# Kernel optimization log

Measured on AMD Instinct MI355X. Metric: run time of the kernel, lower is better.

Reference implementation:

```python
import jax, jax.numpy as jnp
import numpy as np

# TT-linear: in_features=1024 -> out_features=4096
IN_DIMS = (8, 8, 4, 4)      # m1..m4, prod = 1024
OUT_DIMS = (8, 8, 8, 8)     # n1..n4, prod = 4096
RANKS = (1, 16, 16, 16, 1)  # r0..r4
IN_FEATURES = 1024
OUT_FEATURES = 4096
BATCH, SEQ = 4, 1024


def _init_core(key, shape):
    # uniform(-1,1)/sqrt(fan_in-ish), matching the original's uniform-style init scale
    fan = shape[0] * shape[1]
    return (2.0 * jax.random.uniform(key, shape, dtype=jnp.float32) - 1.0) / np.sqrt(fan).astype(np.float32)


def setup_inputs() -> dict:
    key = jax.random.key(0)
    ks = jax.random.split(key, 6)
    x = jax.random.normal(ks[0], (BATCH, SEQ, IN_FEATURES), dtype=jnp.float32)
    core0 = _init_core(ks[1], (1, 8, 8, 16))    # [r0, m1, n1, r1]
    core1 = _init_core(ks[2], (16, 8, 8, 16))   # [r1, m2, n2, r2]
    core2 = _init_core(ks[3], (16, 4, 8, 16))   # [r2, m3, n3, r3]
    core3 = _init_core(ks[4], (16, 4, 8, 1))    # [r3, m4, n4, r4]
    bias = (2.0 * jax.random.uniform(ks[5], (OUT_FEATURES,), dtype=jnp.float32) - 1.0) / np.sqrt(OUT_FEATURES).astype(np.float32)
    return {"x": x, "core0": core0, "core1": core1, "core2": core2, "core3": core3, "bias": bias}


def reference(x, core0, core1, core2, core3, bias):
    lead = x.shape[:-1]
    # split the feature axis into TT input factors: [T, m1, m2, m3, m4]
    t = x.reshape((-1,) + IN_DIMS)
    c0 = core0[0]        # [m1, n1, r1]   (boundary rank r0 = 1 squeezed)
    c3 = core3[..., 0]   # [r3, m4, n4]   (boundary rank r4 = 1 squeezed)
    # sequential TT core chain: absorb one m_k, emit one n_k per step
    t = jnp.einsum('tijkl,ixp->tjklxp', t, c0)      # [T, m2,m3,m4, n1, r1]
    t = jnp.einsum('tjklxp,pjyq->tklxyq', t, core1)  # [T, m3,m4, n1,n2, r2]
    t = jnp.einsum('tklxyq,qkzr->tlxyzr', t, core2)  # [T, m4, n1,n2,n3, r3]
    t = jnp.einsum('tlxyzr,rlw->txyzw', t, c3)       # [T, n1,n2,n3,n4]
    y = t.reshape(lead + (OUT_FEATURES,)) + bias
    return y
```

## Files before the change

kernel.cpp:

```cpp
#include <hip/hip_runtime.h>
#include <hip/hip_bf16.h>
#include <cstdint>


typedef __bf16 bf16x8 __attribute__((ext_vector_type(8)));
typedef float f32x4 __attribute__((ext_vector_type(4)));

__device__ __forceinline__ void g2lds16(const void* g, void* l) {
    __builtin_amdgcn_global_load_lds(
        (const __attribute__((address_space(1))) void*)g,
        (__attribute__((address_space(3))) void*)l,
        16, 0, 0);
}

__global__ void f32_to_bf16(const float* __restrict__ x, __bf16* __restrict__ y) {
    int i = (blockIdx.x * blockDim.x + threadIdx.x) * 8;
    float4 a = *(const float4*)(x + i);
    float4 b = *(const float4*)(x + i + 4);
    bf16x8 o;
    o[0] = (__bf16)a.x; o[1] = (__bf16)a.y; o[2] = (__bf16)a.z; o[3] = (__bf16)a.w;
    o[4] = (__bf16)b.x; o[5] = (__bf16)b.y; o[6] = (__bf16)b.z; o[7] = (__bf16)b.w;
    *(bf16x8*)(y + i) = o;
}

__global__ void build_wt(const float* __restrict__ c0, const float* __restrict__ c1,
                         const float* __restrict__ c2, const float* __restrict__ c3,
                         __bf16* __restrict__ wt) {
    __shared__ float t12[16];
    __shared__ float t123[4 * 8 * 16];
    const int b = blockIdx.x;
    const int m1 = b >> 9, n1 = (b >> 6) & 7, m2 = (b >> 3) & 7, n2 = b & 7;
    const int tid = threadIdx.x;
    if (tid < 16) {
        const int r2 = tid;
        float s = 0.f;
        #pragma unroll
        for (int r1 = 0; r1 < 16; ++r1)
            s += c0[(m1 * 8 + n1) * 16 + r1] * c1[((r1 * 8 + m2) * 8 + n2) * 16 + r2];
        t12[r2] = s;
    }
    __syncthreads();
    #pragma unroll
    for (int idx = tid; idx < 512; idx += 64) {
        const int m3 = idx >> 7, n3 = (idx >> 4) & 7, r3 = idx & 15;
        float s = 0.f;
        #pragma unroll
        for (int r2 = 0; r2 < 16; ++r2)
            s += t12[r2] * c2[((r2 * 4 + m3) * 8 + n3) * 16 + r3];
        t123[idx] = s;
    }
    __syncthreads();
    #pragma unroll
    for (int idx = tid; idx < 1024; idx += 64) {
        const int m3 = idx >> 8, m4 = (idx >> 6) & 3, n3 = (idx >> 3) & 7, n4 = idx & 7;
        float s = 0.f;
        #pragma unroll
        for (int r3 = 0; r3 < 16; ++r3)
            s += t123[(m3 * 8 + n3) * 16 + r3] * c3[(r3 * 4 + m4) * 8 + n4];
        const int k = ((m1 * 8 + m2) * 4 + m3) * 4 + m4;
        const int n = ((n1 * 8 + n2) * 8 + n3) * 8 + n4;
        wt[n * 1024 + k] = (__bf16)s;
    }
}

__global__ __launch_bounds__(256) void tt_gemm(
    const __bf16* __restrict__ A, const __bf16* __restrict__ B,
    const float* __restrict__ bias, float* __restrict__ C) {
    constexpr int K = 1024, N = 4096;
    __shared__ __bf16 sA[128 * 64];
    __shared__ __bf16 sB[128 * 64];
    const int t = threadIdx.x;
    const int lane = t & 63;
    const int wave = t >> 6;
    const int wm = (wave >> 1) * 64;
    const int wn = (wave & 1) * 64;
    const int bm = (blockIdx.x >> 5) * 128;
    const int bn = (blockIdx.x & 31) * 128;
    const int l15 = lane & 15, lh = lane >> 4;

    f32x4 acc[4][4] = {};

    for (int k0 = 0; k0 < K; k0 += 64) {
        __syncthreads();
        #pragma unroll
        for (int i = 0; i < 4; ++i) {
            const int c = t + i * 256;
            const int r = c >> 3;
            const int col = (c & 7) * 8;
            g2lds16(A + (size_t)(bm + r) * K + k0 + col, (char*)sA + (size_t)c * 16);
            g2lds16(B + (size_t)(bn + r) * K + k0 + col, (char*)sB + (size_t)c * 16);
        }
        asm volatile("s_waitcnt vmcnt(0)" ::: "memory");
        __syncthreads();
        #pragma unroll
        for (int kk = 0; kk < 2; ++kk) {
            bf16x8 af[4], bfr[4];
            #pragma unroll
            for (int mi = 0; mi < 4; ++mi)
                af[mi] = *(const bf16x8*)&sA[(wm + mi * 16 + l15) * 64 + kk * 32 + lh * 8];
            #pragma unroll
            for (int ni = 0; ni < 4; ++ni)
                bfr[ni] = *(const bf16x8*)&sB[(wn + ni * 16 + l15) * 64 + kk * 32 + lh * 8];
            #pragma unroll
            for (int mi = 0; mi < 4; ++mi)
                #pragma unroll
                for (int ni = 0; ni < 4; ++ni)
                    acc[mi][ni] = __builtin_amdgcn_mfma_f32_16x16x32_bf16(
                        af[mi], bfr[ni], acc[mi][ni], 0, 0, 0);
        }
    }

    #pragma unroll
    for (int ni = 0; ni < 4; ++ni) {
        const int col = bn + wn + ni * 16 + l15;
        const float bv = bias[col];
        #pragma unroll
        for (int mi = 0; mi < 4; ++mi) {
            const int row0 = bm + wm + mi * 16 + lh * 4;
            const f32x4 v = acc[mi][ni];
            #pragma unroll
            for (int r = 0; r < 4; ++r)
                C[(size_t)(row0 + r) * N + col] = v[r] + bv;
        }
    }
}

extern "C" void kernel_launch(void* const* d_in, const int* in_sizes, int n_in,
                              void* d_out, int out_size, void* d_ws, size_t ws_size,
                              hipStream_t stream) {
    const float* x    = (const float*)d_in[0];
    const float* c0   = (const float*)d_in[1];
    const float* c1   = (const float*)d_in[2];
    const float* c2   = (const float*)d_in[3];
    const float* c3   = (const float*)d_in[4];
    const float* bias = (const float*)d_in[5];
    float* out = (float*)d_out;

    __bf16* xb = (__bf16*)d_ws;
    __bf16* wt = xb + (size_t)4096 * 1024;

    f32_to_bf16<<<2048, 256, 0, stream>>>(x, xb);
    build_wt<<<4096, 64, 0, stream>>>(c0, c1, c2, c3, wt);
    tt_gemm<<<1024, 256, 0, stream>>>(xb, wt, bias, out);
}
```

Measured before the change: 164.6 us.

## Fuse prep kernels, vectorize weight build, swizzle LDS, remap GEMM tiles per XCD

Merges the fp32→bf16 conversion and the TT weight reconstruction into one launch, packing four weight groups per 256-thread block. Weight writes become 16-element vector stores along K instead of scattered scalar stores, and core3 is staged in LDS. The GEMM gets an XOR swizzle on LDS rows to cut bank conflicts on fragment reads. It also remaps block IDs so each XCD works on a contiguous slice of N for better L2 reuse. Costs are more indexing logic and a heavier prep kernel that could become imbalanced.

```diff
diff --git a/kernel.cpp b/kernel.cpp
--- a/kernel.cpp
+++ b/kernel.cpp
@@ -13,54 +13,73 @@
         16, 0, 0);
 }
 
-__global__ void f32_to_bf16(const float* __restrict__ x, __bf16* __restrict__ y) {
-    int i = (blockIdx.x * blockDim.x + threadIdx.x) * 8;
-    float4 a = *(const float4*)(x + i);
-    float4 b = *(const float4*)(x + i + 4);
-    bf16x8 o;
-    o[0] = (__bf16)a.x; o[1] = (__bf16)a.y; o[2] = (__bf16)a.z; o[3] = (__bf16)a.w;
-    o[4] = (__bf16)b.x; o[5] = (__bf16)b.y; o[6] = (__bf16)b.z; o[7] = (__bf16)b.w;
-    *(bf16x8*)(y + i) = o;
-}
-
-__global__ void build_wt(const float* __restrict__ c0, const float* __restrict__ c1,
-                         const float* __restrict__ c2, const float* __restrict__ c3,
-                         __bf16* __restrict__ wt) {
-    __shared__ float t12[16];
-    __shared__ float t123[4 * 8 * 16];
+__global__ __launch_bounds__(256) void prep(
+    const float* __restrict__ x, __bf16* __restrict__ xb,
+    const float* __restrict__ c0, const float* __restrict__ c1,
+    const float* __restrict__ c2, const float* __restrict__ c3,
+    __bf16* __restrict__ wt) {
     const int b = blockIdx.x;
-    const int m1 = b >> 9, n1 = (b >> 6) & 7, m2 = (b >> 3) & 7, n2 = b & 7;
-    const int tid = threadIdx.x;
-    if (tid < 16) {
-        const int r2 = tid;
-        float s = 0.f;
+    const int t = threadIdx.x;
+    if (b < 2048) {
+        const int i = (b * 256 + t) * 8;
+        float4 a0 = *(const float4*)(x + i);
+        float4 a1 = *(const float4*)(x + i + 4);
+        bf16x8 o;
+        o[0] = (__bf16)a0.x; o[1] = (__bf16)a0.y; o[2] = (__bf16)a0.z; o[3] = (__bf16)a0.w;
+        o[4] = (__bf16)a1.x; o[5] = (__bf16)a1.y; o[6] = (__bf16)a1.z; o[7] = (__bf16)a1.w;
+        *(bf16x8*)(xb + i) = o;
+        return;
+    }
+    __shared__ float t12[4][16];
+    __shared__ float t123[4][512];
+    __shared__ float c3s[512];
+    #pragma unroll
+    for (int i = t; i < 512; i += 256) c3s[i] = c3[i];
+    const int s = t >> 6;
+    const int lane = t & 63;
+    const int g = (b - 2048) * 4 + s;
+    const int m1 = g >> 9, n1 = (g >> 6) & 7, m2 = (g >> 3) & 7, n2 = g & 7;
+    __syncthreads();
+    if (lane < 16) {
+        const int r2 = lane;
+        float sum = 0.f;
         #pragma unroll
         for (int r1 = 0; r1 < 16; ++r1)
-            s += c0[(m1 * 8 + n1) * 16 + r1] * c1[((r1 * 8 + m2) * 8 + n2) * 16 + r2];
-        t12[r2] = s;
+            sum += c0[(m1 * 8 + n1) * 16 + r1] * c1[((r1 * 8 + m2) * 8 + n2) * 16 + r2];
+        t12[s][r2] = sum;
     }
     __syncthreads();
     #pragma unroll
-    for (int idx = tid; idx < 512; idx += 64) {
+    for (int idx = lane; idx < 512; idx += 64) {
         const int m3 = idx >> 7, n3 = (idx >> 4) & 7, r3 = idx & 15;
-        float s = 0.f;
+        float sum = 0.f;
         #pragma unroll
         for (int r2 = 0; r2 < 16; ++r2)
-            s += t12[r2] * c2[((r2 * 4 + m3) * 8 + n3) * 16 + r3];
-        t123[idx] = s;
+            sum += t12[s][r2] * c2[((r2 * 4 + m3) * 8 + n3) * 16 + r3];
+        t123[s][(m3 * 8 + n3) * 16 + r3] = sum;
     }
     __syncthreads();
+    const int n3 = lane >> 3, n4 = lane & 7;
+    const int n = ((n1 * 8 + n2) * 8 + n3) * 8 + n4;
+    const int kbase = (m1 * 8 + m2) * 16;
+    float v[16];
     #pragma unroll
-    for (int idx = tid; idx < 1024; idx += 64) {
-        const int m3 = idx >> 8, m4 = (idx >> 6) & 3, n3 = (idx >> 3) & 7, n4 = idx & 7;
-        float s = 0.f;
+    for (int e = 0; e < 16; ++e) v[e] = 0.f;
+    #pragma unroll
+    for (int m3 = 0; m3 < 4; ++m3) {
         #pragma unroll
-        for (int r3 = 0; r3 < 16; ++r3)
-            s += t123[(m3 * 8 + n3) * 16 + r3] * c3[(r3 * 4 + m4) * 8 + n4];
-        const int k = ((m1 * 8 + m2) * 4 + m3) * 4 + m4;
-        const int n = ((n1 * 8 + n2) * 8 + n3) * 8 + n4;
-        wt[n * 1024 + k] = (__bf16)s;
+        for (int r3 = 0; r3 < 16; ++r3) {
+            const float tv = t123[s][(m3 * 8 + n3) * 16 + r3];
+            #pragma unroll
+            for (int m4 = 0; m4 < 4; ++m4)
+                v[m3 * 4 + m4] += tv * c3s[(r3 * 4 + m4) * 8 + n4];
+        }
     }
+    bf16x8 lo, hi;
+    #pragma unroll
+    for (int e = 0; e < 8; ++e) { lo[e] = (__bf16)v[e]; hi[e] = (__bf16)v[8 + e]; }
+    *(bf16x8*)(wt + (size_t)n * 1024 + kbase)     = lo;
+    *(bf16x8*)(wt + (size_t)n * 1024 + kbase + 8) = hi;
 }
 
 __global__ __launch_bounds__(256) void tt_gemm(
@@ -74,9 +93,12 @@
     const int wave = t >> 6;
     const int wm = (wave >> 1) * 64;
     const int wn = (wave & 1) * 64;
-    const int bm = (blockIdx.x >> 5) * 128;
-    const int bn = (blockIdx.x & 31) * 128;
+    const int xcd = blockIdx.x & 7;
+    const int lid = blockIdx.x >> 3;
+    const int bm = (lid & 31) * 128;
+    const int bn = (xcd * 4 + (lid >> 5)) * 128;
     const int l15 = lane & 15, lh = lane >> 4;
+    const int swz = l15 & 7;
 
     f32x4 acc[4][4] = {};
 
@@ -86,21 +108,22 @@
         for (int i = 0; i < 4; ++i) {
             const int c = t + i * 256;
             const int r = c >> 3;
-            const int col = (c & 7) * 8;
-            g2lds16(A + (size_t)(bm + r) * K + k0 + col, (char*)sA + (size_t)c * 16);
-            g2lds16(B + (size_t)(bn + r) * K + k0 + col, (char*)sB + (size_t)c * 16);
+            const int gc = (c & 7) ^ (r & 7);
+            g2lds16(A + (size_t)(bm + r) * K + k0 + gc * 8, (char*)sA + (size_t)c * 16);
+            g2lds16(B + (size_t)(bn + r) * K + k0 + gc * 8, (char*)sB + (size_t)c * 16);
         }
         asm volatile("s_waitcnt vmcnt(0)" ::: "memory");
         __syncthreads();
         #pragma unroll
         for (int kk = 0; kk < 2; ++kk) {
+            const int coff = ((kk * 4 + lh) ^ swz) * 16;
             bf16x8 af[4], bfr[4];
             #pragma unroll
             for (int mi = 0; mi < 4; ++mi)
-                af[mi] = *(const bf16x8*)&sA[(wm + mi * 16 + l15) * 64 + kk * 32 + lh * 8];
+                af[mi] = *(const bf16x8*)((const char*)sA + (size_t)(wm + mi * 16 + l15) * 128 + coff);
             #pragma unroll
             for (int ni = 0; ni < 4; ++ni)
-                bfr[ni] = *(const bf16x8*)&sB[(wn + ni * 16 + l15) * 64 + kk * 32 + lh * 8];
+                bfr[ni] = *(const bf16x8*)((const char*)sB + (size_t)(wn + ni * 16 + l15) * 128 + coff);
             #pragma unroll
             for (int mi = 0; mi < 4; ++mi)
                 #pragma unroll
@@ -139,7 +162,6 @@
     __bf16* xb = (__bf16*)d_ws;
     __bf16* wt = xb + (size_t)4096 * 1024;
 
-    f32_to_bf16<<<2048, 256, 0, stream>>>(x, xb);
-    build_wt<<<4096, 64, 0, stream>>>(c0, c1, c2, c3, wt);
+    prep<<<3072, 256, 0, stream>>>(x, xb, c0, c1, c2, c3, wt);
     tt_gemm<<<1024, 256, 0, stream>>>(xb, wt, bias, out);
 }
```

New measurement: 142.1 us. 1.16x faster.
